# Kernel tuning notes

Measured on AMD Instinct MI355X. Metric: run time of the kernel, lower is better.

## Reference

```python
import jax, jax.numpy as jnp
import numpy as np

NODE_DIM = 64
EDGE_DIM = 16
HIDDEN = 64
INPUT_DIM = 2 * NODE_DIM + EDGE_DIM  # 144
NEG_SLOPE = 0.1
LN_EPS = 1e-5


def _layer_norm(x, gamma, beta):
    mu = jnp.mean(x, axis=-1, keepdims=True)
    var = jnp.var(x, axis=-1, keepdims=True)
    return (x - mu) * jax.lax.rsqrt(var + LN_EPS) * gamma + beta


def _leaky_relu(x):
    return jnp.where(x >= 0, x, NEG_SLOPE * x)


def setup_inputs() -> dict:
    key = jax.random.key(0)
    ks = jax.random.split(key, 10)
    n_nodes, n_edges = 50000, 1600000
    node_features = jax.random.normal(ks[0], (n_nodes, NODE_DIM), dtype=jnp.float32)
    edge_index = jax.random.randint(ks[1], (2, n_edges), 0, n_nodes, dtype=jnp.int64)
    edge_attr = jax.random.normal(ks[2], (n_edges, EDGE_DIM), dtype=jnp.float32)
    # MLP parameters (kaiming-ish scale)
    W1 = jax.random.normal(ks[3], (INPUT_DIM, HIDDEN), dtype=jnp.float32) / np.sqrt(INPUT_DIM)
    b1 = jnp.zeros((HIDDEN,), dtype=jnp.float32)
    g1 = jnp.ones((HIDDEN,), dtype=jnp.float32)
    be1 = jnp.zeros((HIDDEN,), dtype=jnp.float32)
    W2 = jax.random.normal(ks[4], (HIDDEN, HIDDEN), dtype=jnp.float32) / np.sqrt(HIDDEN)
    b2 = jnp.zeros((HIDDEN,), dtype=jnp.float32)
    g2 = jnp.ones((HIDDEN,), dtype=jnp.float32)
    be2 = jnp.zeros((HIDDEN,), dtype=jnp.float32)
    W3 = jax.random.normal(ks[5], (HIDDEN, 1), dtype=jnp.float32) / np.sqrt(HIDDEN)
    b3 = jnp.zeros((1,), dtype=jnp.float32)
    return {
        "node_features": node_features, "edge_index": edge_index, "edge_attr": edge_attr,
        "W1": W1, "b1": b1, "g1": g1, "be1": be1,
        "W2": W2, "b2": b2, "g2": g2, "be2": be2,
        "W3": W3, "b3": b3,
    }


def reference(node_features, edge_index, edge_attr,
              W1, b1, g1, be1, W2, b2, g2, be2, W3, b3):
    src = node_features[edge_index[0]]  # (E, node_dim)
    dst = node_features[edge_index[1]]  # (E, node_dim)
    x = jnp.concatenate([src, dst, edge_attr], axis=-1)  # (E, input_dim)
    h = _leaky_relu(_layer_norm(x @ W1 + b1, g1, be1))
    h = _leaky_relu(_layer_norm(h @ W2 + b2, g2, be2))
    return (h @ W3 + b3)[:, 0]  # (E,) logits
```

## Files before the change

### kernel.cpp

```cpp
#include <hip/hip_runtime.h>
#include <stdint.h>


#define TPB 256
#define NEG_SLOPE 0.1f
#define LN_EPS    1e-5f

typedef __attribute__((ext_vector_type(8))) short short8;
typedef __attribute__((ext_vector_type(4))) float f32x4;

__device__ __forceinline__ uint32_t fb(float x) {
  union { float f; uint32_t u; } c; c.f = x; return c.u;
}
__device__ __forceinline__ float bf(uint32_t x) {
  union { uint32_t u; float f; } c; c.u = x; return c.f;
}
__device__ __forceinline__ uint32_t pkbf(float a, float b) {
  return __builtin_amdgcn_perm(fb(b) + 0x8000u, fb(a) + 0x8000u, 0x07060302u);
}
__device__ __forceinline__ short8 cvt8(f32x4 a, f32x4 b) {
  union { short8 s; uint32_t u[4]; } r;
  r.u[0] = pkbf(a[0], a[1]);
  r.u[1] = pkbf(a[2], a[3]);
  r.u[2] = pkbf(b[0], b[1]);
  r.u[3] = pkbf(b[2], b[3]);
  return r.s;
}
__device__ __forceinline__ short bf16rne(float x) {
  uint32_t u = fb(x);
  return (short)((u + 0x7fffu + ((u >> 16) & 1u)) >> 16);
}

template <int CTRL>
__device__ __forceinline__ float dppadd(float v) {
  int r = __builtin_amdgcn_update_dpp(0, (int)fb(v), CTRL, 0xf, 0xf, true);
  return v + bf((uint32_t)r);
}
__device__ __forceinline__ float rowsum16(float v) {
  v = dppadd<0x121>(v);
  v = dppadd<0x122>(v);
  v = dppadd<0x124>(v);
  v = dppadd<0x128>(v);
  return v;
}
__device__ __forceinline__ void redsum16(f32x4& v) {
  #pragma unroll
  for (int c = 0; c < 4; ++c) v[c] = rowsum16(v[c]);
}

__global__ __launch_bounds__(TPB, 2)
void edge_mlp_mfma(const float* __restrict__ nf, const int* __restrict__ ei,
                   const float* __restrict__ ea,
                   const float* __restrict__ W1, const float* __restrict__ b1,
                   const float* __restrict__ g1, const float* __restrict__ be1,
                   const float* __restrict__ W2, const float* __restrict__ b2,
                   const float* __restrict__ g2, const float* __restrict__ be2,
                   const float* __restrict__ W3, const float* __restrict__ b3,
                   float* __restrict__ out, int E, int ntiles) {
  __shared__ short W1T[64 * 168];
  __shared__ short W2T[64 * 72];
  __shared__ short HB[4][16 * 72];

  const int tid  = threadIdx.x;
  const int lane = tid & 63;
  const int wv   = tid >> 6;
  const int ln   = lane & 15;
  const int quad = lane >> 4;

  for (int i = tid; i < 9216; i += TPB) {
    int n = i & 63, k = i >> 6;
    W1T[n * 168 + k] = bf16rne(W1[k * 64 + n]);
  }
  for (int i = tid; i < 1024; i += TPB) {
    int n = i & 63, k = 144 + (i >> 6);
    W1T[n * 168 + k] = 0;
  }
  for (int i = tid; i < 4096; i += TPB) {
    int n = i & 63, k = i >> 6;
    W2T[n * 72 + k] = bf16rne(W2[k * 64 + n]);
  }
  __syncthreads();

  float b1v[4], g1v[4], be1v[4], b2v[4], g2v[4], be2v[4], W3v[4];
  #pragma unroll
  for (int jt = 0; jt < 4; ++jt) {
    int n = ln + 16 * jt;
    b1v[jt] = b1[n];  g1v[jt] = g1[n];  be1v[jt] = be1[n];
    b2v[jt] = b2[n];  g2v[jt] = g2[n];  be2v[jt] = be2[n];
    W3v[jt] = W3[n];
  }
  const float b3s = b3[0];

  const bool idx64 = (__ballot(ei[2 * lane + 1] == 0) == ~0ull);

  int sI[4], dI[4], eC[4];
  {
    const int ebase = blockIdx.x * 256 + wv * 64;
    #pragma unroll
    for (int mt = 0; mt < 4; ++mt) {
      int el = ebase + mt * 16 + ln;
      int ec = el < E ? el : E - 1;
      eC[mt] = ec;
      if (idx64) { sI[mt] = ei[2 * ec]; dI[mt] = ei[2 * (E + ec)]; }
      else       { sI[mt] = ei[ec];     dI[mt] = ei[E + ec]; }
    }
  }

  for (int tile = blockIdx.x; tile < ntiles; tile += gridDim.x) {
    const int ebase = tile * 256 + wv * 64;

    short8 afr[4][5];
    #pragma unroll
    for (int mt = 0; mt < 4; ++mt) {
      const float* sp = nf + (size_t)sI[mt] * 64 + quad * 8;
      const float* dp = nf + (size_t)dI[mt] * 64 + quad * 8;
      const float* ap = ea + (size_t)eC[mt] * 16 + (quad & 1) * 8;
      f32x4 c0 = *(const f32x4*)sp;        f32x4 c1 = *(const f32x4*)(sp + 4);
      f32x4 c2 = *(const f32x4*)(sp + 32); f32x4 c3 = *(const f32x4*)(sp + 36);
      f32x4 c4 = *(const f32x4*)dp;        f32x4 c5 = *(const f32x4*)(dp + 4);
      f32x4 c6 = *(const f32x4*)(dp + 32); f32x4 c7 = *(const f32x4*)(dp + 36);
      f32x4 c8 = *(const f32x4*)ap;        f32x4 c9 = *(const f32x4*)(ap + 4);
      afr[mt][0] = cvt8(c0, c1);
      afr[mt][1] = cvt8(c2, c3);
      afr[mt][2] = cvt8(c4, c5);
      afr[mt][3] = cvt8(c6, c7);
      afr[mt][4] = cvt8(c8, c9);
    }

    f32x4 acc[4][4];
    #pragma unroll
    for (int mt = 0; mt < 4; ++mt)
      #pragma unroll
      for (int jt = 0; jt < 4; ++jt) acc[mt][jt] = (f32x4)(b1v[jt]);

    #pragma unroll
    for (int t = 0; t < 5; ++t)
      #pragma unroll
      for (int jt = 0; jt < 4; ++jt) {
        short8 bfr = *(const short8*)&W1T[(jt * 16 + ln) * 168 + t * 32 + quad * 8];
        #pragma unroll
        for (int mt = 0; mt < 4; ++mt)
          acc[mt][jt] = __builtin_amdgcn_mfma_f32_16x16x32_bf16(
              afr[mt][t], bfr, acc[mt][jt], 0, 0, 0);
      }

    {
      int ntile = tile + gridDim.x;
      if (ntile < ntiles) {
        const int nb = ntile * 256 + wv * 64;
        #pragma unroll
        for (int mt = 0; mt < 4; ++mt) {
          int el = nb + mt * 16 + ln;
          int ec = el < E ? el : E - 1;
          eC[mt] = ec;
          if (idx64) { sI[mt] = ei[2 * ec]; dI[mt] = ei[2 * (E + ec)]; }
          else       { sI[mt] = ei[ec];     dI[mt] = ei[E + ec]; }
        }
      }
    }

    #pragma unroll
    for (int mt = 0; mt < 4; ++mt) {
      f32x4 sv = acc[mt][0] + acc[mt][1] + acc[mt][2] + acc[mt][3];
      f32x4 qv = acc[mt][0] * acc[mt][0] + acc[mt][1] * acc[mt][1]
               + acc[mt][2] * acc[mt][2] + acc[mt][3] * acc[mt][3];
      redsum16(sv);
      redsum16(qv);
      f32x4 mu  = sv * (1.f / 64.f);
      f32x4 var = qv * (1.f / 64.f) - mu * mu;
      f32x4 rs;
      rs[0] = rsqrtf(var[0] + LN_EPS); rs[1] = rsqrtf(var[1] + LN_EPS);
      rs[2] = rsqrtf(var[2] + LN_EPS); rs[3] = rsqrtf(var[3] + LN_EPS);

      #pragma unroll
      for (int jt = 0; jt < 4; ++jt)
        #pragma unroll
        for (int r = 0; r < 4; ++r) {
          float h = (acc[mt][jt][r] - mu[r]) * rs[r] * g1v[jt] + be1v[jt];
          h = fmaxf(h, NEG_SLOPE * h);
          HB[wv][(quad * 4 + r) * 72 + ln + 16 * jt] =
              (short)((fb(h) + 0x8000u) >> 16);
        }
      asm volatile("s_waitcnt lgkmcnt(0)" ::: "memory");

      f32x4 acc2[4];
      #pragma unroll
      for (int jt = 0; jt < 4; ++jt) acc2[jt] = (f32x4)(b2v[jt]);
      #pragma unroll
      for (int t2 = 0; t2 < 2; ++t2) {
        short8 a2 = *(const short8*)&HB[wv][ln * 72 + t2 * 32 + quad * 8];
        #pragma unroll
        for (int jt = 0; jt < 4; ++jt) {
          short8 w2f = *(const short8*)&W2T[(jt * 16 + ln) * 72 + t2 * 32 + quad * 8];
          acc2[jt] = __builtin_amdgcn_mfma_f32_16x16x32_bf16(
              a2, w2f, acc2[jt], 0, 0, 0);
        }
      }

      f32x4 s2 = acc2[0] + acc2[1] + acc2[2] + acc2[3];
      f32x4 q2 = acc2[0] * acc2[0] + acc2[1] * acc2[1]
               + acc2[2] * acc2[2] + acc2[3] * acc2[3];
      redsum16(s2);
      redsum16(q2);
      f32x4 mu2  = s2 * (1.f / 64.f);
      f32x4 var2 = q2 * (1.f / 64.f) - mu2 * mu2;
      f32x4 rs2;
      rs2[0] = rsqrtf(var2[0] + LN_EPS); rs2[1] = rsqrtf(var2[1] + LN_EPS);
      rs2[2] = rsqrtf(var2[2] + LN_EPS); rs2[3] = rsqrtf(var2[3] + LN_EPS);

      f32x4 po = (f32x4)0.f;
      #pragma unroll
      for (int jt = 0; jt < 4; ++jt)
        #pragma unroll
        for (int r = 0; r < 4; ++r) {
          float h = (acc2[jt][r] - mu2[r]) * rs2[r] * g2v[jt] + be2v[jt];
          h = fmaxf(h, NEG_SLOPE * h);
          po[r] = fmaf(h, W3v[jt], po[r]);
        }
      redsum16(po);

      if (ln < 4) {
        int e = ebase + mt * 16 + quad * 4 + ln;
        if (e < E) {
          float v = (ln == 0) ? po[0] : (ln == 1) ? po[1] : (ln == 2) ? po[2] : po[3];
          out[e] = v + b3s;
        }
      }
    }
  }
}

extern "C" void kernel_launch(void* const* d_in, const int* in_sizes, int n_in,
                              void* d_out, int out_size, void* d_ws, size_t ws_size,
                              hipStream_t stream) {
  const float* nf = (const float*)d_in[0];
  const int*   ei = (const int*)d_in[1];
  const float* ea = (const float*)d_in[2];

  const int E = out_size;
  const int ntiles = (E + 255) / 256;
  const int blocks = ntiles < 1024 ? ntiles : 1024;

  edge_mlp_mfma<<<blocks, TPB, 0, stream>>>(
      nf, ei, ea,
      (const float*)d_in[3],  (const float*)d_in[4],
      (const float*)d_in[5],  (const float*)d_in[6],
      (const float*)d_in[7],  (const float*)d_in[8],
      (const float*)d_in[9],  (const float*)d_in[10],
      (const float*)d_in[11], (const float*)d_in[12],
      (float*)d_out, E, ntiles);
}
```

Before: 322.7 us.

## Software-pipeline gathers per 16-edge subtile and raise occupancy to 4 blocks

```diff
diff --git a/kernel.cpp b/kernel.cpp
--- a/kernel.cpp
+++ b/kernel.cpp
@@ -48,7 +48,7 @@
   for (int c = 0; c < 4; ++c) v[c] = rowsum16(v[c]);
 }
 
-__global__ __launch_bounds__(TPB, 2)
+__global__ __launch_bounds__(TPB, 4)
 void edge_mlp_mfma(const float* __restrict__ nf, const int* __restrict__ ei,
                    const float* __restrict__ ea,
                    const float* __restrict__ W1, const float* __restrict__ b1,
@@ -93,77 +93,79 @@
 
   const bool idx64 = (__ballot(ei[2 * lane + 1] == 0) == ~0ull);
 
-  int sI[4], dI[4], eC[4];
+  int sI[4], dI[4], sN[4], dN[4];
   {
-    const int ebase = blockIdx.x * 256 + wv * 64;
+    const int eb0 = blockIdx.x * 256 + wv * 64;
     #pragma unroll
     for (int mt = 0; mt < 4; ++mt) {
-      int el = ebase + mt * 16 + ln;
+      int el = eb0 + mt * 16 + ln;
       int ec = el < E ? el : E - 1;
-      eC[mt] = ec;
       if (idx64) { sI[mt] = ei[2 * ec]; dI[mt] = ei[2 * (E + ec)]; }
       else       { sI[mt] = ei[ec];     dI[mt] = ei[E + ec]; }
+      sN[mt] = sI[mt]; dN[mt] = dI[mt];
     }
   }
+
+  f32x4 raw[10];
+  auto issue = [&](int s, int d, int el) {
+    int ec = el < E ? el : E - 1;
+    const float* sp = nf + (size_t)s * 64 + quad * 8;
+    const float* dp = nf + (size_t)d * 64 + quad * 8;
+    const float* ap = ea + (size_t)ec * 16 + (quad & 1) * 8;
+    raw[0] = *(const f32x4*)sp;        raw[1] = *(const f32x4*)(sp + 4);
+    raw[2] = *(const f32x4*)(sp + 32); raw[3] = *(const f32x4*)(sp + 36);
+    raw[4] = *(const f32x4*)dp;        raw[5] = *(const f32x4*)(dp + 4);
+    raw[6] = *(const f32x4*)(dp + 32); raw[7] = *(const f32x4*)(dp + 36);
+    raw[8] = *(const f32x4*)ap;        raw[9] = *(const f32x4*)(ap + 4);
+  };
+
+  issue(sI[0], dI[0], blockIdx.x * 256 + wv * 64 + ln);
 
   for (int tile = blockIdx.x; tile < ntiles; tile += gridDim.x) {
     const int ebase = tile * 256 + wv * 64;
 
-    short8 afr[4][5];
     #pragma unroll
     for (int mt = 0; mt < 4; ++mt) {
-      const float* sp = nf + (size_t)sI[mt] * 64 + quad * 8;
-      const float* dp = nf + (size_t)dI[mt] * 64 + quad * 8;
-      const float* ap = ea + (size_t)eC[mt] * 16 + (quad & 1) * 8;
-      f32x4 c0 = *(const f32x4*)sp;        f32x4 c1 = *(const f32x4*)(sp + 4);
-      f32x4 c2 = *(const f32x4*)(sp + 32); f32x4 c3 = *(const f32x4*)(sp + 36);
-      f32x4 c4 = *(const f32x4*)dp;        f32x4 c5 = *(const f32x4*)(dp + 4);
-      f32x4 c6 = *(const f32x4*)(dp + 32); f32x4 c7 = *(const f32x4*)(dp + 36);
-      f32x4 c8 = *(const f32x4*)ap;        f32x4 c9 = *(const f32x4*)(ap + 4);
-      afr[mt][0] = cvt8(c0, c1);
-      afr[mt][1] = cvt8(c2, c3);
-      afr[mt][2] = cvt8(c4, c5);
-      afr[mt][3] = cvt8(c6, c7);
-      afr[mt][4] = cvt8(c8, c9);
-    }
-
-    f32x4 acc[4][4];
-    #pragma unroll
-    for (int mt = 0; mt < 4; ++mt)
-      #pragma unroll
-      for (int jt = 0; jt < 4; ++jt) acc[mt][jt] = (f32x4)(b1v[jt]);
-
-    #pragma unroll
-    for (int t = 0; t < 5; ++t)
-      #pragma unroll
-      for (int jt = 0; jt < 4; ++jt) {
-        short8 bfr = *(const short8*)&W1T[(jt * 16 + ln) * 168 + t * 32 + quad * 8];
-        #pragma unroll
-        for (int mt = 0; mt < 4; ++mt)
-          acc[mt][jt] = __builtin_amdgcn_mfma_f32_16x16x32_bf16(
-              afr[mt][t], bfr, acc[mt][jt], 0, 0, 0);
+      short8 afr[5];
+      afr[0] = cvt8(raw[0], raw[1]);
+      afr[1] = cvt8(raw[2], raw[3]);
+      afr[2] = cvt8(raw[4], raw[5]);
+      afr[3] = cvt8(raw[6], raw[7]);
+      afr[4] = cvt8(raw[8], raw[9]);
+
+      f32x4 acc[4];
+      #pragma unroll
+      for (int jt = 0; jt < 4; ++jt) acc[jt] = (f32x4)(b1v[jt]);
+
+      #pragma unroll
+      for (int t = 0; t < 5; ++t)
+        #pragma unroll
+        for (int jt = 0; jt < 4; ++jt) {
+          short8 bfr = *(const short8*)&W1T[(jt * 16 + ln) * 168 + t * 32 + quad * 8];
+          acc[jt] = __builtin_amdgcn_mfma_f32_16x16x32_bf16(
+              afr[t], bfr, acc[jt], 0, 0, 0);
+        }
+
+      if (mt == 1) {
+        int ntile = tile + gridDim.x;
+        if (ntile < ntiles) {
+          const int nb = ntile * 256 + wv * 64;
+          #pragma unroll
+          for (int m2 = 0; m2 < 4; ++m2) {
+            int el = nb + m2 * 16 + ln;
+            int ec = el < E ? el : E - 1;
+            if (idx64) { sN[m2] = ei[2 * ec]; dN[m2] = ei[2 * (E + ec)]; }
+            else       { sN[m2] = ei[ec];     dN[m2] = ei[E + ec]; }
+          }
+        }
       }
 
-    {
-      int ntile = tile + gridDim.x;
-      if (ntile < ntiles) {
-        const int nb = ntile * 256 + wv * 64;
-        #pragma unroll
-        for (int mt = 0; mt < 4; ++mt) {
-          int el = nb + mt * 16 + ln;
-          int ec = el < E ? el : E - 1;
-          eC[mt] = ec;
-          if (idx64) { sI[mt] = ei[2 * ec]; dI[mt] = ei[2 * (E + ec)]; }
-          else       { sI[mt] = ei[ec];     dI[mt] = ei[E + ec]; }
-        }
-      }
-    }
-
-    #pragma unroll
-    for (int mt = 0; mt < 4; ++mt) {
-      f32x4 sv = acc[mt][0] + acc[mt][1] + acc[mt][2] + acc[mt][3];
-      f32x4 qv = acc[mt][0] * acc[mt][0] + acc[mt][1] * acc[mt][1]
-               + acc[mt][2] * acc[mt][2] + acc[mt][3] * acc[mt][3];
+      if (mt < 3) issue(sI[mt + 1], dI[mt + 1], ebase + (mt + 1) * 16 + ln);
+      else        issue(sN[0], dN[0], (tile + (int)gridDim.x) * 256 + wv * 64 + ln);
+
+      f32x4 sv = acc[0] + acc[1] + acc[2] + acc[3];
+      f32x4 qv = acc[0] * acc[0] + acc[1] * acc[1]
+               + acc[2] * acc[2] + acc[3] * acc[3];
       redsum16(sv);
       redsum16(qv);
       f32x4 mu  = sv * (1.f / 64.f);
@@ -176,7 +178,7 @@
       for (int jt = 0; jt < 4; ++jt)
         #pragma unroll
         for (int r = 0; r < 4; ++r) {
-          float h = (acc[mt][jt][r] - mu[r]) * rs[r] * g1v[jt] + be1v[jt];
+          float h = (acc[jt][r] - mu[r]) * rs[r] * g1v[jt] + be1v[jt];
           h = fmaxf(h, NEG_SLOPE * h);
           HB[wv][(quad * 4 + r) * 72 + ln + 16 * jt] =
               (short)((fb(h) + 0x8000u) >> 16);
@@ -227,6 +229,9 @@
         }
       }
     }
+
+    #pragma unroll
+    for (int m2 = 0; m2 < 4; ++m2) { sI[m2] = sN[m2]; dI[m2] = dN[m2]; }
   }
 }
 
@@ -239,7 +244,7 @@
 
   const int E = out_size;
   const int ntiles = (E + 255) / 256;
-  const int blocks = ntiles < 1024 ? ntiles : 1024;
+  const int blocks = ntiles < 2048 ? ntiles : 2048;
 
   edge_mlp_mfma<<<blocks, TPB, 0, stream>>>(
       nf, ei, ea,
```

New measurement: 395.3 us. +22.5%, slower.
